# Kernel tuning notes

Hardware: AMD Instinct MI355X
Metric: run time of the kernel (lower is better)

The kernel has to match this reference:

```python
import jax, jax.numpy as jnp
import numpy as np

B, S, D, H = 4, 2048, 1024, 16
DEPTH = D // H


def setup_inputs() -> dict:
    key = jax.random.key(0)
    ks = jax.random.split(key, 12)
    q = jax.random.normal(ks[0], (B, S, D), dtype=jnp.float32)
    k = jax.random.normal(ks[1], (B, S, D), dtype=jnp.float32)
    v = jax.random.normal(ks[2], (B, S, D), dtype=jnp.float32)
    # causal mask: 1.0 where attention is disallowed (upper triangle), per `mask * -1e9`
    mask = 1.0 - jnp.tril(jnp.ones((S, S), dtype=jnp.float32))
    mask = mask[None, None, :, :]  # [1,1,S,S] broadcastable over batch/heads
    scale = 1.0 / np.sqrt(D)
    Wq = jax.random.normal(ks[3], (D, D), dtype=jnp.float32) * scale
    Wk = jax.random.normal(ks[4], (D, D), dtype=jnp.float32) * scale
    Wv = jax.random.normal(ks[5], (D, D), dtype=jnp.float32) * scale
    Wo = jax.random.normal(ks[6], (D, D), dtype=jnp.float32) * scale
    bq = jnp.zeros((D,), jnp.float32)
    bk = jnp.zeros((D,), jnp.float32)
    bv = jnp.zeros((D,), jnp.float32)
    bo = jnp.zeros((D,), jnp.float32)
    return {"query": q, "key": k, "value": v, "mask": mask,
            "Wq": Wq, "bq": bq, "Wk": Wk, "bk": bk,
            "Wv": Wv, "bv": bv, "Wo": Wo, "bo": bo}


def _split_heads(x):
    # [B, S, D] -> [B, H, S, depth]
    b, s, _ = x.shape
    return x.reshape(b, s, H, DEPTH).transpose(0, 2, 1, 3)


def reference(query, key, value, mask, Wq, bq, Wk, bk, Wv, bv, Wo, bo):
    q = _split_heads(query @ Wq + bq)   # [B,H,S,depth]
    k = _split_heads(key @ Wk + bk)
    v = _split_heads(value @ Wv + bv)
    scores = jnp.einsum('bhqd,bhkd->bhqk', q, k) / jnp.sqrt(
        jnp.asarray(DEPTH, q.dtype))
    scores = scores + mask * (-1e9)
    attn = jax.nn.softmax(scores, axis=-1)
    out = jnp.einsum('bhqk,bhkd->bhqd', attn, v)   # [B,H,S,depth]
    out = out.transpose(0, 2, 1, 3).reshape(query.shape[0], -1, H * DEPTH)
    return out @ Wo + bo
```

## Files before the change

kernel.cpp:

```cpp
#include <hip/hip_runtime.h>

#define Bsz 4
#define SEQ 2048
#define DIM 1024
#define NH 16
#define HD 64

typedef float  f32x4  __attribute__((ext_vector_type(4)));
typedef __bf16 bf16x8 __attribute__((ext_vector_type(8)));
typedef __bf16 bf16x4 __attribute__((ext_vector_type(4)));
typedef short  s16x4  __attribute__((ext_vector_type(4)));

__device__ __forceinline__ f32x4 mfma16(bf16x8 a, bf16x8 b, f32x4 c) {
    return __builtin_amdgcn_mfma_f32_16x16x32_bf16(a, b, c, 0, 0, 0);
}
__device__ __forceinline__ f32x4 mfma16k16(bf16x4 a, bf16x4 b, f32x4 c) {
#if defined(__has_builtin) && __has_builtin(__builtin_amdgcn_mfma_f32_16x16x16bf16_1k)
    return __builtin_amdgcn_mfma_f32_16x16x16bf16_1k(
        __builtin_bit_cast(s16x4, a), __builtin_bit_cast(s16x4, b), c, 0, 0, 0);
#else
    asm volatile("s_nop 2\n\tv_mfma_f32_16x16x16_bf16 %0, %1, %2, %0\n\ts_nop 7\n\ts_nop 7"
                 : "+v"(c) : "v"(a), "v"(b));
    return c;
#endif
}

__device__ __forceinline__ float fast_exp2(float x) {
#if defined(__has_builtin) && __has_builtin(__builtin_amdgcn_exp2f)
    return __builtin_amdgcn_exp2f(x);
#else
    return exp2f(x);
#endif
}

#define GLD_LDS16(gsrc, ldst)                                                        \
    __builtin_amdgcn_global_load_lds(                                                \
        (const __attribute__((address_space(1))) void*)(gsrc),                       \
        (__attribute__((address_space(3))) void*)(ldst), 16, 0, 0)

__global__ __launch_bounds__(256) void wt_kernel(
    const float* __restrict__ Wq, const float* __restrict__ Wk,
    const float* __restrict__ Wv, const float* __restrict__ Wo,
    __bf16* __restrict__ wt)
{
    __shared__ float tile[64][65];
    int z = blockIdx.z;
    const float* W = (z == 0) ? Wq : (z == 1) ? Wk : (z == 2) ? Wv : Wo;
    __bf16* out = wt + (size_t)z * DIM * DIM;
    int kb = blockIdx.x * 64, nb = blockIdx.y * 64;
    int t = threadIdx.x;
    int cidx = t & 63, ridx = t >> 6;
#pragma unroll
    for (int i = 0; i < 16; i++) {
        int r = ridx + i * 4;
        tile[r][cidx] = W[(size_t)(kb + r) * DIM + nb + cidx];
    }
    __syncthreads();
#pragma unroll
    for (int i = 0; i < 16; i++) {
        int r = ridx + i * 4;
        out[(size_t)(nb + r) * DIM + kb + cidx] = (__bf16)tile[cidx][r];
    }
}

__global__ __launch_bounds__(256, 2) void gemm_proj(
    const float* __restrict__ Xq, const float* __restrict__ Xk,
    const float* __restrict__ Xv, const __bf16* __restrict__ wt,
    const float* __restrict__ bq, const float* __restrict__ bk,
    const float* __restrict__ bv,
    __bf16* __restrict__ oq, __bf16* __restrict__ ok, __bf16* __restrict__ ovT)
{
    int z = blockIdx.z;
    const float*  X    = (z == 0) ? Xq : (z == 1) ? Xk : Xv;
    const float*  bias = (z == 0) ? bq : (z == 1) ? bk : bv;
    const __bf16* Bt   = wt + (size_t)z * DIM * DIM;

    __shared__ __align__(16) char smem[49152];
    float*  const Af = (float*)smem;
    __bf16* const Bb = (__bf16*)(smem + 32768);

    int m0 = blockIdx.x * 128, n0 = blockIdx.y * 128;
    int tid = threadIdx.x, lane = tid & 63, w = tid >> 6;
    int c = lane & 15, g = lane >> 4;
    int wm = (w >> 1) * 64, wn = (w & 1) * 64;

    f32x4 acc[4][4] = {};

    int ar = tid >> 3, ach = tid & 7;
    int asch = ach ^ (ar & 7);
    const float* aptr = X + (size_t)(m0 + ar) * DIM + asch * 4;
    int srow = (w * 2) * 16 + (lane >> 2);
    int scol = (lane & 3) * 8;
    const __bf16* bptr0 = Bt + (size_t)(n0 + srow) * DIM + scol;
    const __bf16* bptr1 = bptr0 + (size_t)16 * DIM;
    int so0 = (w * 2) * 512;
    int so1 = (w * 2 + 1) * 512;

#define STAGE_PROJ(buf, k0)                                                      \
    do {                                                                         \
        GLD_LDS16(aptr + (k0),                     Af + (buf) * 4096 + w * 256); \
        GLD_LDS16(aptr + (k0) + (size_t)32 * DIM,  Af + (buf) * 4096 + 1024 + w * 256); \
        GLD_LDS16(aptr + (k0) + (size_t)64 * DIM,  Af + (buf) * 4096 + 2048 + w * 256); \
        GLD_LDS16(aptr + (k0) + (size_t)96 * DIM,  Af + (buf) * 4096 + 3072 + w * 256); \
        GLD_LDS16(bptr0 + (k0),                    Bb + (buf) * 4096 + so0);     \
        GLD_LDS16(bptr1 + (k0),                    Bb + (buf) * 4096 + so1);     \
    } while (0)

    STAGE_PROJ(0, 0);
    __syncthreads();

    int cur = 0;
    for (int kt = 0; kt < 32; ++kt) {
        int nxt = kt + 1;
        int nb = cur ^ 1;
        if (nxt < 32) STAGE_PROJ(nb, nxt * 32);

        bf16x8 af[4], bf[4];
#pragma unroll
        for (int mf = 0; mf < 4; mf++) {
            int arow = wm + mf * 16 + c;
            const float* ap = &Af[cur * 4096 + arow * 32];
            f32x4 a0 = *(const f32x4*)(ap + (((2 * g)     ^ (c & 7)) << 2));
            f32x4 a1 = *(const f32x4*)(ap + (((2 * g + 1) ^ (c & 7)) << 2));
            bf16x8 v;
#pragma unroll
            for (int j = 0; j < 4; j++) { v[j] = (__bf16)a0[j]; v[4 + j] = (__bf16)a1[j]; }
            af[mf] = v;
        }
#pragma unroll
        for (int nf = 0; nf < 4; nf++)
            bf[nf] = *(bf16x8*)&Bb[cur * 4096 + (wn + nf * 16 + c) * 32 + g * 8];
#pragma unroll
        for (int mf = 0; mf < 4; mf++)
#pragma unroll
            for (int nf = 0; nf < 4; nf++)
                acc[mf][nf] = mfma16(af[mf], bf[nf], acc[mf][nf]);
        __syncthreads();
        cur = nb;
    }
#undef STAGE_PROJ

    if (z == 2) {
        __bf16* T = (__bf16*)smem + (size_t)w * 2304;
        int h = (n0 + wn) >> 6;
        int bb = m0 >> 11;
        int s_base = (m0 & (SEQ - 1)) + wm;
        int dd = lane >> 2;
        int ss = (lane & 3) * 8;
        size_t obase = ((size_t)(bb * NH + h) * HD) * SEQ;
#pragma unroll
        for (int half = 0; half < 2; half++) {
#pragma unroll
            for (int mh = 0; mh < 2; mh++) {
                int mf = half * 2 + mh;
#pragma unroll
                for (int nf = 0; nf < 4; nf++) {
                    int col = n0 + wn + nf * 16 + c;
                    int d = nf * 16 + c;
                    float bval = bias[col];
                    bf16x4 pk;
#pragma unroll
                    for (int r = 0; r < 4; r++) pk[r] = (__bf16)(acc[mf][nf][r] + bval);
                    *(bf16x4*)&T[d * 36 + mh * 16 + g * 4] = pk;
                }
            }
#pragma unroll
            for (int dgrp = 0; dgrp < 4; dgrp++) {
                int d = dgrp * 16 + dd;
                bf16x8 vv = *(bf16x8*)&T[d * 36 + ss];
                *(bf16x8*)&ovT[obase + (size_t)d * SEQ + s_base + half * 32 + ss] = vv;
            }
        }
    } else {
        __bf16* Out = (z == 0) ? oq : ok;
#pragma unroll
        for (int nf = 0; nf < 4; nf++) {
            int col = n0 + wn + nf * 16 + c;
            float bval = bias[col];
#pragma unroll
            for (int mf = 0; mf < 4; mf++) {
                int row = m0 + wm + mf * 16 + g * 4;
#pragma unroll
                for (int r = 0; r < 4; r++)
                    Out[(size_t)(row + r) * DIM + col] = (__bf16)(acc[mf][nf][r] + bval);
            }
        }
    }
}

#define QSCALE 0.180336880f

__global__ __launch_bounds__(256, 2) void fa_kernel(
    const __bf16* __restrict__ qp, const __bf16* __restrict__ kp,
    const __bf16* __restrict__ vpT, __bf16* __restrict__ op)
{
    int bz = blockIdx.x;
    int bh = bz & 63;
    int b = bh >> 4, h = bh & 15;
    int qt = 31 - (bz >> 6);
    int q0 = qt * 64;

    int tid = threadIdx.x, lane = tid & 63, w = tid >> 6;
    int c = lane & 15, g = lane >> 4;

    __shared__ __bf16 Kbuf[64 * 64];
    __shared__ __bf16 Vbuf[64 * 64];

    const int qg = q0 + w * 16 + c;

    bf16x8 qf[2];
    {
        const __bf16* qbase = qp + (size_t)(b * SEQ + qg) * DIM + h * HD;
#pragma unroll
        for (int kc = 0; kc < 2; kc++) {
            bf16x8 raw = *(const bf16x8*)(qbase + kc * 32 + g * 8);
            bf16x8 sc;
#pragma unroll
            for (int j = 0; j < 8; j++) sc[j] = (__bf16)((float)raw[j] * QSCALE);
            qf[kc] = sc;
        }
    }

    f32x4 acc[4] = {};
    float m_run = -1e30f;
    float l_run = 0.f;

    int r8 = tid >> 3, c8 = tid & 7;
    int sch = c8 ^ (r8 & 7);
    const __bf16* kbase = kp  + (size_t)(b * SEQ + r8) * DIM + h * HD + sch * 8;
    const __bf16* vbase = vpT + ((size_t)(b * NH + h) * HD + r8) * SEQ + sch * 8;
    __bf16* kdst0 = Kbuf + w * 512;
    __bf16* kdst1 = Kbuf + 2048 + w * 512;
    __bf16* vdst0 = Vbuf + w * 512;
    __bf16* vdst1 = Vbuf + 2048 + w * 512;

    int vb4[4];
#pragma unroll
    for (int mkey = 0; mkey < 4; mkey++)
        vb4[mkey] = c * 64 + (((2 * mkey + (g >> 1)) ^ (c & 7)) * 8) + (g & 1) * 4;

    int ktmax = qt + 1;
    for (int kt = 0; kt < ktmax; ++kt) {
        GLD_LDS16(kbase + (size_t)kt * 64 * DIM, kdst0);
        GLD_LDS16(kbase + (size_t)(kt * 64 + 32) * DIM, kdst1);
        GLD_LDS16(vbase + kt * 64, vdst0);
        GLD_LDS16(vbase + kt * 64 + (size_t)32 * SEQ, vdst1);
        __syncthreads();

        int kb0 = kt * 64;

        f32x4 s[4] = {};
        __builtin_amdgcn_s_setprio(1);
#pragma unroll
        for (int kc = 0; kc < 2; kc++) {
            bf16x8 kf[4];
#pragma unroll
            for (int mkey = 0; mkey < 4; mkey++)
                kf[mkey] = *(bf16x8*)&Kbuf[(mkey * 16 + c) * 64 + (((kc * 4 + g) ^ (c & 7)) * 8)];
#pragma unroll
            for (int mkey = 0; mkey < 4; mkey++)
                s[mkey] = mfma16(kf[mkey], qf[kc], s[mkey]);
        }
        __builtin_amdgcn_s_setprio(0);

        if (kb0 + 63 > qg) {
#pragma unroll
            for (int mkey = 0; mkey < 4; mkey++)
#pragma unroll
                for (int r2 = 0; r2 < 4; r2++)
                    if (kb0 + mkey * 16 + g * 4 + r2 > qg) s[mkey][r2] = -1e30f;
        }

        float pm = fmaxf(fmaxf(s[0][0], s[0][1]), s[0][2]);
        pm = fmaxf(fmaxf(pm, s[0][3]), s[1][0]);
        pm = fmaxf(fmaxf(pm, s[1][1]), s[1][2]);
        pm = fmaxf(fmaxf(pm, s[1][3]), s[2][0]);
        pm = fmaxf(fmaxf(pm, s[2][1]), s[2][2]);
        pm = fmaxf(fmaxf(pm, s[2][3]), s[3][0]);
        pm = fmaxf(fmaxf(pm, s[3][1]), s[3][2]);
        pm = fmaxf(pm, s[3][3]);
        pm = fmaxf(pm, __shfl_xor(pm, 16));
        pm = fmaxf(pm, __shfl_xor(pm, 32));
        if (!__all(pm <= m_run + 8.f)) {
            float mn = fmaxf(m_run, pm);
            float scl = fast_exp2(m_run - mn);
            l_run *= scl;
#pragma unroll
            for (int nf = 0; nf < 4; nf++) acc[nf] *= scl;
            m_run = mn;
        }
        f32x4 rsv = {0.f, 0.f, 0.f, 0.f};
        bf16x4 pf[4];
#pragma unroll
        for (int mkey = 0; mkey < 4; mkey++) {
            bf16x4 pk;
#pragma unroll
            for (int r2 = 0; r2 < 4; r2++) {
                float p = fast_exp2(s[mkey][r2] - m_run);
                rsv[r2] += p;
                pk[r2] = (__bf16)p;
            }
            pf[mkey] = pk;
        }
        float rs = (rsv[0] + rsv[1]) + (rsv[2] + rsv[3]);
        rs += __shfl_xor(rs, 16);
        rs += __shfl_xor(rs, 32);
        l_run += rs;

        __builtin_amdgcn_s_setprio(1);
#pragma unroll
        for (int mkey = 0; mkey < 4; mkey++) {
#pragma unroll
            for (int nf = 0; nf < 4; nf++) {
                bf16x4 vf = *(bf16x4*)&Vbuf[vb4[mkey] + nf * 1024];
                acc[nf] = mfma16k16(vf, pf[mkey], acc[nf]);
            }
        }
        __builtin_amdgcn_s_setprio(0);
        __syncthreads();
    }

    {
        float inv = 1.f / l_run;
        __bf16* obase = op + (size_t)(b * SEQ + qg) * DIM + h * HD + g * 4;
#pragma unroll
        for (int nf = 0; nf < 4; nf++) {
            bf16x4 pk;
#pragma unroll
            for (int r2 = 0; r2 < 4; r2++) pk[r2] = (__bf16)(acc[nf][r2] * inv);
            *(bf16x4*)(obase + nf * 16) = pk;
        }
    }
}

__global__ __launch_bounds__(256, 2) void gemm_out(
    const __bf16* __restrict__ Ain, const __bf16* __restrict__ wt,
    const float* __restrict__ bias, float* __restrict__ Out)
{
    const __bf16* Bt = wt + (size_t)3 * DIM * DIM;

    __shared__ __bf16 Ab[2][4096];
    __shared__ __bf16 Bb[2][4096];

    int m0 = blockIdx.x * 128, n0 = blockIdx.y * 128;
    int tid = threadIdx.x, lane = tid & 63, w = tid >> 6;
    int c = lane & 15, g = lane >> 4;
    int wm = (w >> 1) * 64, wn = (w & 1) * 64;

    f32x4 acc[4][4] = {};

    int srow = (w * 2) * 16 + (lane >> 2);
    int scol = (lane & 3) * 8;
    const __bf16* aptr0 = Ain + (size_t)(m0 + srow) * DIM + scol;
    const __bf16* aptr1 = aptr0 + (size_t)16 * DIM;
    const __bf16* bptr0 = Bt + (size_t)(n0 + srow) * DIM + scol;
    const __bf16* bptr1 = bptr0 + (size_t)16 * DIM;
    int so0 = (w * 2) * 512;
    int so1 = (w * 2 + 1) * 512;

    GLD_LDS16(aptr0, Ab[0] + so0);
    GLD_LDS16(aptr1, Ab[0] + so1);
    GLD_LDS16(bptr0, Bb[0] + so0);
    GLD_LDS16(bptr1, Bb[0] + so1);
    __syncthreads();

    int cur = 0;
    for (int kt = 0; kt < 32; ++kt) {
        int nxt = kt + 1;
        int nb = cur ^ 1;
        if (nxt < 32) {
            int k0 = nxt * 32;
            GLD_LDS16(aptr0 + k0, Ab[nb] + so0);
            GLD_LDS16(aptr1 + k0, Ab[nb] + so1);
            GLD_LDS16(bptr0 + k0, Bb[nb] + so0);
            GLD_LDS16(bptr1 + k0, Bb[nb] + so1);
        }
        bf16x8 af[4], bf[4];
#pragma unroll
        for (int mf = 0; mf < 4; mf++)
            af[mf] = *(bf16x8*)&Ab[cur][(wm + mf * 16 + c) * 32 + g * 8];
#pragma unroll
        for (int nf = 0; nf < 4; nf++)
            bf[nf] = *(bf16x8*)&Bb[cur][(wn + nf * 16 + c) * 32 + g * 8];
#pragma unroll
        for (int mf = 0; mf < 4; mf++)
#pragma unroll
            for (int nf = 0; nf < 4; nf++)
                acc[mf][nf] = mfma16(af[mf], bf[nf], acc[mf][nf]);
        __syncthreads();
        cur = nb;
    }

#pragma unroll
    for (int nf = 0; nf < 4; nf++) {
        int col = n0 + wn + nf * 16 + c;
        float bval = bias[col];
#pragma unroll
        for (int mf = 0; mf < 4; mf++) {
            int row = m0 + wm + mf * 16 + g * 4;
#pragma unroll
            for (int r = 0; r < 4; r++)
                Out[(size_t)(row + r) * DIM + col] = acc[mf][nf][r] + bval;
        }
    }
}

extern "C" void kernel_launch(void* const* d_in, const int* in_sizes, int n_in,
                              void* d_out, int out_size, void* d_ws, size_t ws_size,
                              hipStream_t stream)
{
    const float* q  = (const float*)d_in[0];
    const float* k  = (const float*)d_in[1];
    const float* v  = (const float*)d_in[2];
    const float* Wq = (const float*)d_in[4];
    const float* bq = (const float*)d_in[5];
    const float* Wk = (const float*)d_in[6];
    const float* bk = (const float*)d_in[7];
    const float* Wv = (const float*)d_in[8];
    const float* bv = (const float*)d_in[9];
    const float* Wo = (const float*)d_in[10];
    const float* bo = (const float*)d_in[11];

    char* ws = (char*)d_ws;
    __bf16* wt  = (__bf16*)ws;
    __bf16* qp  = (__bf16*)(ws + (size_t)(8u  << 20));
    __bf16* kp  = (__bf16*)(ws + (size_t)(24u << 20));
    __bf16* vpT = (__bf16*)(ws + (size_t)(40u << 20));
    __bf16* ao  = (__bf16*)(ws + (size_t)(56u << 20));

    wt_kernel<<<dim3(16, 16, 4), 256, 0, stream>>>(Wq, Wk, Wv, Wo, wt);
    gemm_proj<<<dim3(64, 8, 3), 256, 0, stream>>>(q, k, v, wt, bq, bk, bv, qp, kp, vpT);
    fa_kernel<<<dim3(2048), 256, 0, stream>>>(qp, kp, vpT, ao);
    gemm_out<<<dim3(64, 8), 256, 0, stream>>>(ao, wt, bo, (float*)d_out);

    (void)in_sizes; (void)n_in; (void)out_size; (void)ws_size;
}
```

Before: 172.5 us.

## Prefetch next K/V tile into registers and defer row-sum reduction

Replaces the direct global-to-LDS loads of each K/V tile with register prefetching of the next tile during compute, then stores it to LDS between two barriers. This is meant to hide global load latency behind the MFMA and softmax work. It also moves the cross-lane row-sum shuffle reduction out of the loop into the epilogue. The cost is extra VGPRs, an extra barrier per iteration, and an LDS write path through registers.

```diff
diff --git a/kernel.cpp b/kernel.cpp
--- a/kernel.cpp
+++ b/kernel.cpp
@@ -229,10 +229,7 @@
     int sch = c8 ^ (r8 & 7);
     const __bf16* kbase = kp  + (size_t)(b * SEQ + r8) * DIM + h * HD + sch * 8;
     const __bf16* vbase = vpT + ((size_t)(b * NH + h) * HD + r8) * SEQ + sch * 8;
-    __bf16* kdst0 = Kbuf + w * 512;
-    __bf16* kdst1 = Kbuf + 2048 + w * 512;
-    __bf16* vdst0 = Vbuf + w * 512;
-    __bf16* vdst1 = Vbuf + 2048 + w * 512;
+    int slot = tid * 8;
 
     int vb4[4];
 #pragma unroll
@@ -240,12 +237,27 @@
         vb4[mkey] = c * 64 + (((2 * mkey + (g >> 1)) ^ (c & 7)) * 8) + (g & 1) * 4;
 
     int ktmax = qt + 1;
+
+    bf16x8 kv0 = *(const bf16x8*)(kbase);
+    bf16x8 kv1 = *(const bf16x8*)(kbase + (size_t)32 * DIM);
+    bf16x8 vv0 = *(const bf16x8*)(vbase);
+    bf16x8 vv1 = *(const bf16x8*)(vbase + (size_t)32 * SEQ);
+    *(bf16x8*)&Kbuf[slot]        = kv0;
+    *(bf16x8*)&Kbuf[2048 + slot] = kv1;
+    *(bf16x8*)&Vbuf[slot]        = vv0;
+    *(bf16x8*)&Vbuf[2048 + slot] = vv1;
+    __syncthreads();
+
     for (int kt = 0; kt < ktmax; ++kt) {
-        GLD_LDS16(kbase + (size_t)kt * 64 * DIM, kdst0);
-        GLD_LDS16(kbase + (size_t)(kt * 64 + 32) * DIM, kdst1);
-        GLD_LDS16(vbase + kt * 64, vdst0);
-        GLD_LDS16(vbase + kt * 64 + (size_t)32 * SEQ, vdst1);
-        __syncthreads();
+        bool more = (kt + 1 < ktmax);
+        if (more) {
+            const __bf16* kn = kbase + (size_t)(kt + 1) * 64 * DIM;
+            const __bf16* vn = vbase + (kt + 1) * 64;
+            kv0 = *(const bf16x8*)(kn);
+            kv1 = *(const bf16x8*)(kn + (size_t)32 * DIM);
+            vv0 = *(const bf16x8*)(vn);
+            vv1 = *(const bf16x8*)(vn + (size_t)32 * SEQ);
+        }
 
         int kb0 = kt * 64;
 
@@ -302,10 +314,7 @@
             }
             pf[mkey] = pk;
         }
-        float rs = (rsv[0] + rsv[1]) + (rsv[2] + rsv[3]);
-        rs += __shfl_xor(rs, 16);
-        rs += __shfl_xor(rs, 32);
-        l_run += rs;
+        l_run += (rsv[0] + rsv[1]) + (rsv[2] + rsv[3]);
 
         __builtin_amdgcn_s_setprio(1);
 #pragma unroll
@@ -317,11 +326,22 @@
             }
         }
         __builtin_amdgcn_s_setprio(0);
+
         __syncthreads();
+        if (more) {
+            *(bf16x8*)&Kbuf[slot]        = kv0;
+            *(bf16x8*)&Kbuf[2048 + slot] = kv1;
+            *(bf16x8*)&Vbuf[slot]        = vv0;
+            *(bf16x8*)&Vbuf[2048 + slot] = vv1;
+        }
+        __syncthreads();
     }
 
     {
-        float inv = 1.f / l_run;
+        float l = l_run;
+        l += __shfl_xor(l, 16);
+        l += __shfl_xor(l, 32);
+        float inv = 1.f / l;
         __bf16* obase = op + (size_t)(b * SEQ + qg) * DIM + h * HD + g * 4;
 #pragma unroll
         for (int nf = 0; nf < 4; nf++) {
```

New measurement: 175.7 us. About the same (+1.9%).
